# Kernel optimization log

Measured on AMD Instinct MI355X. Metric: run time of the kernel, lower is better.

Reference implementation:

```python
import jax, jax.numpy as jnp
import numpy as np


def setup_inputs() -> dict:
    key = jax.random.key(0)
    k1, k2, k3 = jax.random.split(key, 3)
    B, D, C = 16384, 1024, 14
    z_image = jax.random.normal(k1, (B, D), dtype=jnp.float32)
    z_text = jax.random.normal(k2, (B, D), dtype=jnp.float32)
    labels = jax.random.randint(k3, (B, C), 0, 2, dtype=jnp.int32)
    return {"z_image": z_image, "z_text": z_text, "labels": labels}


def _margins(labels):
    # labels: [B, C] binary; imposter index j = (i+1) % B -> roll by -1
    lj = jnp.roll(labels, -1, axis=0)
    equal = jnp.all(labels == lj, axis=1)                     # [B]
    n = jnp.sum(labels | lj, axis=1).astype(jnp.float32)      # union size
    d = jnp.sum(labels ^ lj, axis=1).astype(jnp.float32)      # hamming diff
    m = jnp.where(n > 0, jnp.maximum(0.5, d / jnp.maximum(n, 1.0)), 0.5)
    return jnp.where(equal, 0.0, m)                           # [B]


def reference(z_image, z_text, labels):
    # similarity_function == 'dot' (default path of the torch module)
    margin = _margins(labels)                                  # [B]
    paired = jnp.sum(z_image * z_text, axis=1)                 # dot(img_i, txt_i)
    imp_img = jnp.sum(jnp.roll(z_image, -1, axis=0) * z_text, axis=1)  # dot(img_j, txt_i)
    imp_txt = jnp.sum(jnp.roll(z_text, -1, axis=0) * z_image, axis=1)  # dot(txt_j, img_i)
    loss_img = jnp.mean(jax.nn.relu(imp_img - paired + margin))
    loss_txt = jnp.mean(jax.nn.relu(imp_txt - paired + margin))
    return loss_img + loss_txt
```

## Files before the change

kernel.cpp:

```cpp
#include <hip/hip_runtime.h>


constexpr int D   = 1024;
constexpr int C   = 14;
constexpr int RPB = 16;
constexpr int WPB = 4;

__device__ __forceinline__ float dot4(const float4 x, const float4 y) {
    return x.x * y.x + x.y * y.y + x.z * y.z + x.w * y.w;
}

__global__ __launch_bounds__(256) void rank_phase1(
    const float* __restrict__ zi, const float* __restrict__ zt,
    const int* __restrict__ labels, float* __restrict__ partial, int B)
{
    const int wave = threadIdx.x >> 6;
    const int lane = threadIdx.x & 63;

    const int nwg = gridDim.x;
    const int wg  = (blockIdx.x & 7) * (nwg >> 3) + (blockIdx.x >> 3);

    const int r0  = wg * RPB;
    const int M   = B - 1;
    const int idx = (wave << 6) + lane;

    __shared__ float red[WPB][48];
    __shared__ float mlds[RPB];

    {
        const int kk = lane >> 4, c = lane & 15;
        int lx = 0, lo = 0;
        if (c < C) {
            const int ra = (r0 + 4 * wave + kk) & M;
            const int rb = (ra + 1) & M;
            const int li = labels[(size_t)ra * C + c];
            const int lj = labels[(size_t)rb * C + c];
            lx = li ^ lj;
            lo = li | lj;
        }
        const unsigned long long bx = __ballot(lx != 0);
        const unsigned long long bo = __ballot(lo != 0);
        if (lane < 4) {
            const float dv = (float)__popcll((bx >> (16 * lane)) & 0x3FFFull);
            const float nv = (float)__popcll((bo >> (16 * lane)) & 0x3FFFull);
            mlds[4 * wave + lane] = (dv == 0.f) ? 0.f : fmaxf(0.5f, dv / nv);
        }
    }

    float v[48];
    #pragma unroll
    for (int i = 0; i < 48; ++i) v[i] = 0.f;

    float4 a[5], b[5], na[4], nb[4];
    #pragma unroll
    for (int k = 0; k < 5; ++k) {
        const int r = (r0 + k) & M;
        a[k] = ((const float4*)(zi + (size_t)r * D))[idx];
        b[k] = ((const float4*)(zt + (size_t)r * D))[idx];
    }

    #pragma unroll
    for (int cch = 0; cch < 4; ++cch) {
        if (cch < 3) {
            #pragma unroll
            for (int j = 0; j < 4; ++j) {
                const int r = (r0 + 4 * cch + 5 + j) & M;
                na[j] = ((const float4*)(zi + (size_t)r * D))[idx];
                nb[j] = ((const float4*)(zt + (size_t)r * D))[idx];
            }
        }
        #pragma unroll
        for (int k = 0; k < 4; ++k) {
            v[4 * cch + k]      += dot4(a[k],     b[k]);
            v[16 + 4 * cch + k] += dot4(a[k + 1], b[k]);
            v[32 + 4 * cch + k] += dot4(b[k + 1], a[k]);
        }
        if (cch < 3) {
            a[0] = a[4]; b[0] = b[4];
            #pragma unroll
            for (int j = 0; j < 4; ++j) { a[j + 1] = na[j]; b[j + 1] = nb[j]; }
        }
    }

    #pragma unroll
    for (int off = 32; off > 0; off >>= 1) {
        #pragma unroll
        for (int i = 0; i < 48; ++i) v[i] += __shfl_down(v[i], off, 64);
    }
    if (lane == 0) {
        #pragma unroll
        for (int i = 0; i < 48; ++i) red[wave][i] = v[i];
    }
    __syncthreads();

    if (wave == 0 && lane < RPB) {
        float P = 0.f, I = 0.f, T = 0.f;
        #pragma unroll
        for (int w = 0; w < WPB; ++w) {
            P += red[w][lane];
            I += red[w][16 + lane];
            T += red[w][32 + lane];
        }
        const float m = mlds[lane];
        float local = fmaxf(I - P + m, 0.f) + fmaxf(T - P + m, 0.f);
        #pragma unroll
        for (int off = 8; off > 0; off >>= 1)
            local += __shfl_down(local, off, 16);
        if (lane == 0) partial[wg] = local;
    }
}

__global__ __launch_bounds__(256) void rank_phase2(
    const float* __restrict__ partial, float* __restrict__ out,
    int npart, float invB)
{
    float s = 0.f;
    for (int i = threadIdx.x; i < npart; i += 256) s += partial[i];
    #pragma unroll
    for (int off = 32; off > 0; off >>= 1) s += __shfl_down(s, off, 64);
    __shared__ float sm[4];
    if ((threadIdx.x & 63) == 0) sm[threadIdx.x >> 6] = s;
    __syncthreads();
    if (threadIdx.x == 0)
        out[0] = (sm[0] + sm[1] + sm[2] + sm[3]) * invB;
}

extern "C" void kernel_launch(void* const* d_in, const int* in_sizes, int n_in,
                              void* d_out, int out_size, void* d_ws, size_t ws_size,
                              hipStream_t stream) {
    const float* zi     = (const float*)d_in[0];
    const float* zt     = (const float*)d_in[1];
    const int*   labels = (const int*)d_in[2];
    float*       out    = (float*)d_out;
    float*       ws     = (float*)d_ws;

    const int B      = in_sizes[0] / D;
    const int blocks = B / RPB;

    rank_phase1<<<blocks, 256, 0, stream>>>(zi, zt, labels, ws, B);
    rank_phase2<<<1, 256, 0, stream>>>(ws, out, blocks, 1.0f / (float)B);
}
```

Before: 158.6 us.

## Stage row slabs into LDS via async global_load_lds with double buffering

```diff
diff --git a/kernel.cpp b/kernel.cpp
--- a/kernel.cpp
+++ b/kernel.cpp
@@ -1,13 +1,22 @@
 #include <hip/hip_runtime.h>
 
 
-constexpr int D   = 1024;
-constexpr int C   = 14;
-constexpr int RPB = 16;
-constexpr int WPB = 4;
+constexpr int D     = 1024;
+constexpr int C     = 14;
+constexpr int RPB   = 8;
+constexpr int NR    = RPB + 1;
+constexpr int SW    = 256;
+constexpr int SLABS = D / SW;
+constexpr int WPB   = 4;
 
 __device__ __forceinline__ float dot4(const float4 x, const float4 y) {
     return x.x * y.x + x.y * y.y + x.z * y.z + x.w * y.w;
+}
+
+__device__ __forceinline__ void gl_lds16(const float* g, void* l) {
+    __builtin_amdgcn_global_load_lds(
+        (const __attribute__((address_space(1))) void*)g,
+        (__attribute__((address_space(3))) void*)l, 16, 0, 0);
 }
 
 __global__ __launch_bounds__(256) void rank_phase1(
@@ -19,15 +28,14 @@
 
     const int nwg = gridDim.x;
     const int wg  = (blockIdx.x & 7) * (nwg >> 3) + (blockIdx.x >> 3);
-
     const int r0  = wg * RPB;
     const int M   = B - 1;
-    const int idx = (wave << 6) + lane;
 
-    __shared__ float red[WPB][48];
+    __shared__ float lbuf[2][2 * NR][SW];
     __shared__ float mlds[RPB];
+    __shared__ float red[WPB];
 
-    {
+    if (wave < 2) {
         const int kk = lane >> 4, c = lane & 15;
         int lx = 0, lo = 0;
         if (c < C) {
@@ -46,68 +54,87 @@
             mlds[4 * wave + lane] = (dv == 0.f) ? 0.f : fmaxf(0.5f, dv / nv);
         }
     }
+    asm volatile("s_waitcnt vmcnt(0) lgkmcnt(0)" ::: "memory");
+    __builtin_amdgcn_sched_barrier(0);
 
-    float v[48];
+    const float* gsrc[5];
     #pragma unroll
-    for (int i = 0; i < 48; ++i) v[i] = 0.f;
-
-    float4 a[5], b[5], na[4], nb[4];
-    #pragma unroll
-    for (int k = 0; k < 5; ++k) {
-        const int r = (r0 + k) & M;
-        a[k] = ((const float4*)(zi + (size_t)r * D))[idx];
-        b[k] = ((const float4*)(zt + (size_t)r * D))[idx];
-    }
-
-    #pragma unroll
-    for (int cch = 0; cch < 4; ++cch) {
-        if (cch < 3) {
-            #pragma unroll
-            for (int j = 0; j < 4; ++j) {
-                const int r = (r0 + 4 * cch + 5 + j) & M;
-                na[j] = ((const float4*)(zi + (size_t)r * D))[idx];
-                nb[j] = ((const float4*)(zt + (size_t)r * D))[idx];
-            }
-        }
-        #pragma unroll
-        for (int k = 0; k < 4; ++k) {
-            v[4 * cch + k]      += dot4(a[k],     b[k]);
-            v[16 + 4 * cch + k] += dot4(a[k + 1], b[k]);
-            v[32 + 4 * cch + k] += dot4(b[k + 1], a[k]);
-        }
-        if (cch < 3) {
-            a[0] = a[4]; b[0] = b[4];
-            #pragma unroll
-            for (int j = 0; j < 4; ++j) { a[j + 1] = na[j]; b[j + 1] = nb[j]; }
+    for (int t = 0; t < 5; ++t) {
+        const int i = wave + WPB * t;
+        if (i < 2 * NR) {
+            const int    row = (i < NR) ? i : i - NR;
+            const float* src = (i < NR) ? zi : zt;
+            const int    rg  = (r0 + row) & M;
+            gsrc[t] = src + (size_t)rg * D + 4 * lane;
+        } else {
+            gsrc[t] = nullptr;
         }
     }
 
+    #define STAGE(s)                                                        \
+        {                                                                   \
+            const int _b = (s) & 1;                                         \
+            _Pragma("unroll")                                               \
+            for (int t = 0; t < 5; ++t) {                                   \
+                const int i = wave + WPB * t;                               \
+                if (i < 2 * NR)                                             \
+                    gl_lds16(gsrc[t] + (s) * SW, &lbuf[_b][i][0]);          \
+            }                                                               \
+        }
+
+    const int a = 2 * wave;
+    float p0 = 0.f, p1 = 0.f, i0 = 0.f, i1 = 0.f, t0 = 0.f, t1 = 0.f;
+
+    STAGE(0);
+
+    #pragma unroll
+    for (int s = 0; s < SLABS; ++s) {
+        if (s + 1 < SLABS) {
+            STAGE(s + 1);
+            if (wave < 2) asm volatile("s_waitcnt vmcnt(5)" ::: "memory");
+            else          asm volatile("s_waitcnt vmcnt(4)" ::: "memory");
+        } else {
+            asm volatile("s_waitcnt vmcnt(0)" ::: "memory");
+        }
+        __builtin_amdgcn_s_barrier();
+        __builtin_amdgcn_sched_barrier(0);
+
+        const int b = s & 1;
+        const float4 zia  = ((const float4*)lbuf[b][a])[lane];
+        const float4 zia1 = ((const float4*)lbuf[b][a + 1])[lane];
+        const float4 zia2 = ((const float4*)lbuf[b][a + 2])[lane];
+        const float4 zta  = ((const float4*)lbuf[b][NR + a])[lane];
+        const float4 zta1 = ((const float4*)lbuf[b][NR + a + 1])[lane];
+        const float4 zta2 = ((const float4*)lbuf[b][NR + a + 2])[lane];
+
+        p0 += dot4(zia,  zta);
+        i0 += dot4(zia1, zta);
+        t0 += dot4(zta1, zia);
+        p1 += dot4(zia1, zta1);
+        i1 += dot4(zia2, zta1);
+        t1 += dot4(zta2, zia1);
+
+        __syncthreads();
+    }
+    #undef STAGE
+
     #pragma unroll
     for (int off = 32; off > 0; off >>= 1) {
-        #pragma unroll
-        for (int i = 0; i < 48; ++i) v[i] += __shfl_down(v[i], off, 64);
+        p0 += __shfl_down(p0, off, 64);
+        p1 += __shfl_down(p1, off, 64);
+        i0 += __shfl_down(i0, off, 64);
+        i1 += __shfl_down(i1, off, 64);
+        t0 += __shfl_down(t0, off, 64);
+        t1 += __shfl_down(t1, off, 64);
     }
     if (lane == 0) {
-        #pragma unroll
-        for (int i = 0; i < 48; ++i) red[wave][i] = v[i];
+        const float m0 = mlds[a], m1 = mlds[a + 1];
+        red[wave] = fmaxf(i0 - p0 + m0, 0.f) + fmaxf(t0 - p0 + m0, 0.f)
+                  + fmaxf(i1 - p1 + m1, 0.f) + fmaxf(t1 - p1 + m1, 0.f);
     }
     __syncthreads();
-
-    if (wave == 0 && lane < RPB) {
-        float P = 0.f, I = 0.f, T = 0.f;
-        #pragma unroll
-        for (int w = 0; w < WPB; ++w) {
-            P += red[w][lane];
-            I += red[w][16 + lane];
-            T += red[w][32 + lane];
-        }
-        const float m = mlds[lane];
-        float local = fmaxf(I - P + m, 0.f) + fmaxf(T - P + m, 0.f);
-        #pragma unroll
-        for (int off = 8; off > 0; off >>= 1)
-            local += __shfl_down(local, off, 16);
-        if (lane == 0) partial[wg] = local;
-    }
+    if (threadIdx.x == 0)
+        partial[wg] = red[0] + red[1] + red[2] + red[3];
 }
 
 __global__ __launch_bounds__(256) void rank_phase2(
```

Result: faster. 153.8 us (-3.0%).
